# Optimization experiments

Hardware: AMD Instinct MI355X
Metric: run time of the kernel (lower is better)

The kernel has to match this reference:

```python
import jax, jax.numpy as jnp
import numpy as np


def setup_inputs() -> dict:
    key = jax.random.key(0)
    ks = jax.random.split(key, 8)
    B, E = 1024, 8
    dims = [480, 512, 512, 311]
    inp = {
        "x": jax.random.normal(ks[0], (B, dims[0]), dtype=jnp.float32),
        "weight_blend": jax.random.uniform(ks[1], (E, B), dtype=jnp.float32),
        "w0": jax.random.normal(ks[2], (E, dims[1], dims[0]), dtype=jnp.float32) * 0.05,
        "b0": jax.random.normal(ks[3], (E, dims[1]), dtype=jnp.float32) * 0.05,
        "w1": jax.random.normal(ks[4], (E, dims[2], dims[1]), dtype=jnp.float32) * 0.05,
        "b1": jax.random.normal(ks[5], (E, dims[2]), dtype=jnp.float32) * 0.05,
        "w2": jax.random.normal(ks[6], (E, dims[3], dims[2]), dtype=jnp.float32) * 0.05,
        "b2": jax.random.normal(ks[7], (E, dims[3]), dtype=jnp.float32) * 0.05,
    }
    return inp


def _blend_layer(h, blend, w, b):
    # Original: W_b = sum_e blend[e,b] * w[e]  (materializes [B, d_out, d_in]),
    # then matmul(W_b, h) + bias_b. Fused einsum computes identical math.
    out = jnp.einsum("eb,eoi,bi->bo", blend, w, h)
    out = out + jnp.einsum("eb,eo->bo", blend, b)
    return out


def reference(x, weight_blend, w0, b0, w1, b1, w2, b2):
    # dropout layers are identity (training=False / keep_prob=1)
    h = _blend_layer(x, weight_blend, w0, b0)
    h = jax.nn.elu(h)
    h = _blend_layer(h, weight_blend, w1, b1)
    h = jax.nn.elu(h)
    h = _blend_layer(h, weight_blend, w2, b2)  # no activation on final layer
    return h
```

## Files before the change

kernel.cpp:

```cpp
#include <hip/hip_runtime.h>

typedef __attribute__((ext_vector_type(8))) short short8;
typedef __attribute__((ext_vector_type(4))) float f32x4;

__device__ __forceinline__ unsigned short f2bf(float f) {
    unsigned u = __builtin_bit_cast(unsigned, f);
    unsigned r = (u + 0x7FFFu + ((u >> 16) & 1u)) >> 16;
    return (unsigned short)r;
}
__device__ __forceinline__ float bf2f(unsigned short u) {
    unsigned v = ((unsigned)u) << 16;
    return __builtin_bit_cast(float, v);
}

__device__ __forceinline__ void gload16(const unsigned short* g, unsigned short* l) {
    __builtin_amdgcn_global_load_lds(
        (const __attribute__((address_space(1))) void*)g,
        (__attribute__((address_space(3))) void*)l,
        16, 0, 0);
}

#define WAITV(N) asm volatile("s_waitcnt vmcnt(" #N ")" ::: "memory")
#define BAR() do { asm volatile("" ::: "memory"); __builtin_amdgcn_s_barrier(); asm volatile("" ::: "memory"); } while (0)

__device__ __forceinline__ short8 lds_read_swz(const unsigned short* tile, int row, int colb) {
    int off = row * 64 + colb;
    off ^= ((off >> 7) & 7) << 4;
    return *(const short8*)((const char*)tile + off);
}

__device__ __forceinline__ void cvt_chunk(const float* __restrict__ src,
                                          unsigned short* __restrict__ dst, int t) {
    const float4* s4 = (const float4*)src;
    float4 a = s4[2 * t], b = s4[2 * t + 1];
    union { unsigned short u[8]; int4 v; } r;
    r.u[0] = f2bf(a.x); r.u[1] = f2bf(a.y); r.u[2] = f2bf(a.z); r.u[3] = f2bf(a.w);
    r.u[4] = f2bf(b.x); r.u[5] = f2bf(b.y); r.u[6] = f2bf(b.z); r.u[7] = f2bf(b.w);
    ((int4*)dst)[t] = r.v;
}

__device__ __forceinline__ short8 pack8(float4 a, float4 b) {
    short8 p;
    p[0] = (short)f2bf(a.x); p[1] = (short)f2bf(a.y);
    p[2] = (short)f2bf(a.z); p[3] = (short)f2bf(a.w);
    p[4] = (short)f2bf(b.x); p[5] = (short)f2bf(b.y);
    p[6] = (short)f2bf(b.z); p[7] = (short)f2bf(b.w);
    return p;
}

__global__ __launch_bounds__(512) void k_gemm0(
    const float* __restrict__ A, const float* __restrict__ W,
    const float* __restrict__ blend, const float* __restrict__ bias,
    unsigned short* __restrict__ Y,
    const float* __restrict__ csrc, unsigned short* __restrict__ cdst)
{
    __shared__ unsigned short As[2][4096];
    __shared__ unsigned short Bs[2][4096];

    const int e  = blockIdx.z;
    const int bm = blockIdx.y * 128;
    const int on = blockIdx.x * 128;
    const int t  = threadIdx.x, lane = t & 63, w = t >> 6;
    const int wr = w >> 2, wc = w & 3;

    const int sr = lane >> 2, sce = (lane & 3) * 8;
    const int ra = w * 16 + sr;
    const float* gA = A + (size_t)(bm + ra) * 480 + sce;
    const float* gB = W + ((size_t)e * 512 + (on + ra)) * 480 + sce;

    int woff = ra * 64 + (lane & 3) * 16;
    woff ^= ((woff >> 7) & 7) << 4;

    float4 a0, a1, b0v, b1v;
    a0  = *(const float4*)(gA + 0); a1  = *(const float4*)(gA + 4);
    b0v = *(const float4*)(gB + 0); b1v = *(const float4*)(gB + 4);

    f32x4 acc[4][2] = {};

    for (int kt = 0; kt < 15; ++kt) {
        const int buf = kt & 1;
        *(short8*)((char*)As[buf] + woff) = pack8(a0, a1);
        *(short8*)((char*)Bs[buf] + woff) = pack8(b0v, b1v);
        __syncthreads();

        if (kt < 14) {
            int k0 = (kt + 1) * 32;
            a0  = *(const float4*)(gA + k0);     a1  = *(const float4*)(gA + k0 + 4);
            b0v = *(const float4*)(gB + k0);     b1v = *(const float4*)(gB + k0 + 4);
        }

        short8 af[4], bfr[2];
        #pragma unroll
        for (int fm = 0; fm < 4; ++fm)
            af[fm] = lds_read_swz(As[buf], wr * 64 + fm * 16 + (lane & 15), (lane >> 4) * 16);
        #pragma unroll
        for (int fn = 0; fn < 2; ++fn)
            bfr[fn] = lds_read_swz(Bs[buf], wc * 32 + fn * 16 + (lane & 15), (lane >> 4) * 16);
        #pragma unroll
        for (int fm = 0; fm < 4; ++fm)
            #pragma unroll
            for (int fn = 0; fn < 2; ++fn)
                acc[fm][fn] = __builtin_amdgcn_mfma_f32_16x16x32_bf16(
                    af[fm], bfr[fn], acc[fm][fn], 0, 0, 0);
        __syncthreads();
    }

    const float* blendE = blend + e * 1024;
    const float* biasE  = bias + (size_t)e * 512;
    unsigned short* Ye  = Y + (size_t)e * 1024 * 512;
    #pragma unroll
    for (int fm = 0; fm < 4; ++fm) {
        int i0 = bm + wr * 64 + fm * 16 + (lane >> 4) * 4;
        float4 bl = *(const float4*)&blendE[i0];
        #pragma unroll
        for (int fn = 0; fn < 2; ++fn) {
            int j = on + wc * 32 + fn * 16 + (lane & 15);
            float bs = biasE[j];
            #pragma unroll
            for (int r = 0; r < 4; ++r)
                Ye[(size_t)(i0 + r) * 512 + j] = f2bf((acc[fm][fn][r] + bs) * ((&bl.x)[r]));
        }
    }

    int lb = (blockIdx.z * 8 + blockIdx.y) * 4 + blockIdx.x;
    cvt_chunk(csrc, cdst, lb * 1024 + threadIdx.x);
    cvt_chunk(csrc, cdst, lb * 1024 + 512 + threadIdx.x);
}

__global__ __launch_bounds__(512) void k_gemm(
    const unsigned short* __restrict__ A,
    const unsigned short* __restrict__ W,
    const float* __restrict__ blend, const float* __restrict__ bias,
    unsigned short* __restrict__ Y,
    int K, int N, int ldy,
    const float* __restrict__ csrc, unsigned short* __restrict__ cdst, int nchunk)
{
    __shared__ unsigned short As[3][4096];
    __shared__ unsigned short Bs[3][4096];

    const int e  = blockIdx.z;
    const int bm = blockIdx.y * 128;
    const int on = blockIdx.x * 128;
    const int t  = threadIdx.x, lane = t & 63, w = t >> 6;
    const int wr = w >> 2, wc = w & 3;

    const unsigned short* Wt = W + (size_t)e * N * K;
    const int l2 = lane ^ ((lane >> 3) & 7);
    const int sr = l2 >> 2, sce = (l2 & 3) * 8;
    const int ra = w * 16 + sr;
    int rb = on + ra; if (rb > N - 1) rb = N - 1;
    const unsigned short* gA = A  + (size_t)(bm + ra) * K + sce;
    const unsigned short* gB = Wt + (size_t)rb * K + sce;

    const int ktn = K / 32;

#define STAGE(buf, kt) do { int _k0 = (kt) * 32;                       \
        gload16(gA + _k0, &As[(buf)][w * 512]);                        \
        gload16(gB + _k0, &Bs[(buf)][w * 512]); } while (0)

    f32x4 acc[4][2] = {};
    STAGE(0, 0); STAGE(1, 1); STAGE(2, 2);

    int cur = 0;
    for (int kt = 0; kt < ktn; ++kt) {
        int ahead = ktn - 1 - kt;
        if (ahead >= 2)      WAITV(4);
        else if (ahead == 1) WAITV(2);
        else                 WAITV(0);
        BAR();

        short8 af[4], bfr[2];
        #pragma unroll
        for (int fm = 0; fm < 4; ++fm)
            af[fm] = lds_read_swz(As[cur], wr * 64 + fm * 16 + (lane & 15), (lane >> 4) * 16);
        #pragma unroll
        for (int fn = 0; fn < 2; ++fn)
            bfr[fn] = lds_read_swz(Bs[cur], wc * 32 + fn * 16 + (lane & 15), (lane >> 4) * 16);
        #pragma unroll
        for (int fm = 0; fm < 4; ++fm)
            #pragma unroll
            for (int fn = 0; fn < 2; ++fn)
                acc[fm][fn] = __builtin_amdgcn_mfma_f32_16x16x32_bf16(
                    af[fm], bfr[fn], acc[fm][fn], 0, 0, 0);

        BAR();
        if (kt + 3 < ktn) STAGE(cur, kt + 3);
        cur = (cur == 2) ? 0 : cur + 1;
    }
#undef STAGE

    const float* blendE = blend + e * 1024;
    const float* biasE  = bias + (size_t)e * N;
    unsigned short* Ye  = Y + (size_t)e * 1024 * ldy;
    #pragma unroll
    for (int fm = 0; fm < 4; ++fm) {
        int i0 = bm + wr * 64 + fm * 16 + (lane >> 4) * 4;
        float4 bl = *(const float4*)&blendE[i0];
        #pragma unroll
        for (int fn = 0; fn < 2; ++fn) {
            int j = on + wc * 32 + fn * 16 + (lane & 15);
            if (j < N) {
                float bs = biasE[j];
                #pragma unroll
                for (int r = 0; r < 4; ++r)
                    Ye[(size_t)(i0 + r) * ldy + j] = f2bf((acc[fm][fn][r] + bs) * ((&bl.x)[r]));
            }
        }
    }

    if (cdst) {
        int lb = (blockIdx.z * 8 + blockIdx.y) * gridDim.x + blockIdx.x;
        #pragma unroll
        for (int q = 0; q < 2; ++q) {
            int tl = q * 512 + threadIdx.x;
            if (tl < nchunk) cvt_chunk(csrc, cdst, lb * nchunk + tl);
        }
    }
}

__global__ __launch_bounds__(256) void k_reduce8(
    const unsigned short* __restrict__ Y, unsigned short* __restrict__ out)
{
    int idx = blockIdx.x * 256 + threadIdx.x;
    int b  = idx >> 6;
    int o0 = (idx & 63) * 8;
    size_t base = (size_t)b * 512 + o0;
    float s[8] = {};
    #pragma unroll
    for (int p = 0; p < 8; ++p) {
        int4 v = *(const int4*)&Y[base + (size_t)p * 1024 * 512];
        const unsigned short* u = (const unsigned short*)&v;
        #pragma unroll
        for (int r = 0; r < 8; ++r) s[r] += bf2f(u[r]);
    }
    union { unsigned short u[8]; int4 v; } rr;
    #pragma unroll
    for (int r = 0; r < 8; ++r) {
        float v = (s[r] > 0.f) ? s[r] : expm1f(s[r]);
        rr.u[r] = f2bf(v);
    }
    *(int4*)&out[base] = rr.v;
}

__global__ __launch_bounds__(256) void k_reduce_last(
    const unsigned short* __restrict__ Y, float* __restrict__ out)
{
    int idx = blockIdx.x * 256 + threadIdx.x;
    if (idx >= 1024 * 40) return;
    int b  = idx / 40;
    int o0 = (idx - b * 40) * 8;
    size_t base = (size_t)b * 320 + o0;
    float s[8] = {};
    #pragma unroll
    for (int p = 0; p < 8; ++p) {
        int4 v = *(const int4*)&Y[base + (size_t)p * 1024 * 320];
        const unsigned short* u = (const unsigned short*)&v;
        #pragma unroll
        for (int r = 0; r < 8; ++r) s[r] += bf2f(u[r]);
    }
    #pragma unroll
    for (int r = 0; r < 8; ++r)
        if (o0 + r < 311) out[(size_t)b * 311 + o0 + r] = s[r];
}

extern "C" void kernel_launch(void* const* d_in, const int* in_sizes, int n_in,
                              void* d_out, int out_size, void* d_ws, size_t ws_size,
                              hipStream_t stream) {
    const float* x     = (const float*)d_in[0];
    const float* blend = (const float*)d_in[1];
    const float* w0    = (const float*)d_in[2];
    const float* b0    = (const float*)d_in[3];
    const float* w1    = (const float*)d_in[4];
    const float* b1    = (const float*)d_in[5];
    const float* w2    = (const float*)d_in[6];
    const float* b2    = (const float*)d_in[7];

    char* ws = (char*)d_ws;
    unsigned short* w1b = (unsigned short*)(ws + 0);
    unsigned short* w2b = (unsigned short*)(ws + 4194304);
    unsigned short* h1b = (unsigned short*)(ws + 6742016);
    unsigned short* h2b = (unsigned short*)(ws + 7790592);
    unsigned short* yb  = (unsigned short*)(ws + 8839168);

    k_gemm0<<<dim3(4, 8, 8), 512, 0, stream>>>(x, w0, blend, b0, yb, w1, w1b);
    k_reduce8<<<256, 256, 0, stream>>>(yb, h1b);

    k_gemm<<<dim3(4, 8, 8), 512, 0, stream>>>(h1b, w1b, blend, b1, yb, 512, 512, 512,
                                              w2, w2b, 622);
    k_reduce8<<<256, 256, 0, stream>>>(yb, h2b);

    k_gemm<<<dim3(3, 8, 8), 512, 0, stream>>>(h2b, w2b, blend, b2, yb, 512, 311, 320,
                                              nullptr, nullptr, 0);
    k_reduce_last<<<160, 256, 0, stream>>>(yb, (float*)d_out);
}
```

Baseline: 62.49 us.

## Deepen prefetch pipelines and drop a barrier per K-step in blended GEMMs

New measurement: 54.13 us. 13.4% less time.

```diff
diff --git a/kernel.cpp b/kernel.cpp
--- a/kernel.cpp
+++ b/kernel.cpp
@@ -21,6 +21,7 @@
 }
 
 #define WAITV(N) asm volatile("s_waitcnt vmcnt(" #N ")" ::: "memory")
+#define WAITL0() asm volatile("s_waitcnt lgkmcnt(0)" ::: "memory")
 #define BAR() do { asm volatile("" ::: "memory"); __builtin_amdgcn_s_barrier(); asm volatile("" ::: "memory"); } while (0)
 
 __device__ __forceinline__ short8 lds_read_swz(const unsigned short* tile, int row, int colb) {
@@ -71,24 +72,28 @@
     int woff = ra * 64 + (lane & 3) * 16;
     woff ^= ((woff >> 7) & 7) << 4;
 
-    float4 a0, a1, b0v, b1v;
-    a0  = *(const float4*)(gA + 0); a1  = *(const float4*)(gA + 4);
-    b0v = *(const float4*)(gB + 0); b1v = *(const float4*)(gB + 4);
+    float4 La0[3], La1[3], Lb0[3], Lb1[3];
+    #pragma unroll
+    for (int s = 0; s < 3; ++s) {
+        int k0 = s * 32;
+        La0[s] = *(const float4*)(gA + k0); La1[s] = *(const float4*)(gA + k0 + 4);
+        Lb0[s] = *(const float4*)(gB + k0); Lb1[s] = *(const float4*)(gB + k0 + 4);
+    }
 
     f32x4 acc[4][2] = {};
 
+    #pragma unroll
     for (int kt = 0; kt < 15; ++kt) {
-        const int buf = kt & 1;
-        *(short8*)((char*)As[buf] + woff) = pack8(a0, a1);
-        *(short8*)((char*)Bs[buf] + woff) = pack8(b0v, b1v);
-        __syncthreads();
-
-        if (kt < 14) {
-            int k0 = (kt + 1) * 32;
-            a0  = *(const float4*)(gA + k0);     a1  = *(const float4*)(gA + k0 + 4);
-            b0v = *(const float4*)(gB + k0);     b1v = *(const float4*)(gB + k0 + 4);
-        }
-
+        const int s = kt % 3, buf = kt & 1;
+        *(short8*)((char*)As[buf] + woff) = pack8(La0[s], La1[s]);
+        *(short8*)((char*)Bs[buf] + woff) = pack8(Lb0[s], Lb1[s]);
+        WAITL0();
+        BAR();
+        if (kt + 3 < 15) {
+            int k0 = (kt + 3) * 32;
+            La0[s] = *(const float4*)(gA + k0); La1[s] = *(const float4*)(gA + k0 + 4);
+            Lb0[s] = *(const float4*)(gB + k0); Lb1[s] = *(const float4*)(gB + k0 + 4);
+        }
         short8 af[4], bfr[2];
         #pragma unroll
         for (int fm = 0; fm < 4; ++fm)
@@ -102,7 +107,6 @@
             for (int fn = 0; fn < 2; ++fn)
                 acc[fm][fn] = __builtin_amdgcn_mfma_f32_16x16x32_bf16(
                     af[fm], bfr[fn], acc[fm][fn], 0, 0, 0);
-        __syncthreads();
     }
 
     const float* blendE = blend + e * 1024;
@@ -132,11 +136,11 @@
     const unsigned short* __restrict__ W,
     const float* __restrict__ blend, const float* __restrict__ bias,
     unsigned short* __restrict__ Y,
-    int K, int N, int ldy,
+    int N, int ldy,
     const float* __restrict__ csrc, unsigned short* __restrict__ cdst, int nchunk)
 {
-    __shared__ unsigned short As[3][4096];
-    __shared__ unsigned short Bs[3][4096];
+    __shared__ unsigned short As[4][4096];
+    __shared__ unsigned short Bs[4][4096];
 
     const int e  = blockIdx.z;
     const int bm = blockIdx.y * 128;
@@ -144,49 +148,46 @@
     const int t  = threadIdx.x, lane = t & 63, w = t >> 6;
     const int wr = w >> 2, wc = w & 3;
 
-    const unsigned short* Wt = W + (size_t)e * N * K;
+    const unsigned short* Wt = W + (size_t)e * N * 512;
     const int l2 = lane ^ ((lane >> 3) & 7);
     const int sr = l2 >> 2, sce = (l2 & 3) * 8;
     const int ra = w * 16 + sr;
     int rb = on + ra; if (rb > N - 1) rb = N - 1;
-    const unsigned short* gA = A  + (size_t)(bm + ra) * K + sce;
-    const unsigned short* gB = Wt + (size_t)rb * K + sce;
-
-    const int ktn = K / 32;
+    const unsigned short* gA = A  + (size_t)(bm + ra) * 512 + sce;
+    const unsigned short* gB = Wt + (size_t)rb * 512 + sce;
 
 #define STAGE(buf, kt) do { int _k0 = (kt) * 32;                       \
         gload16(gA + _k0, &As[(buf)][w * 512]);                        \
         gload16(gB + _k0, &Bs[(buf)][w * 512]); } while (0)
 
+#define COMPUTE(cur) do {                                                          \
+        short8 af[4], bfr[2];                                                      \
+        _Pragma("unroll")                                                          \
+        for (int fm = 0; fm < 4; ++fm)                                             \
+            af[fm] = lds_read_swz(As[(cur)], wr * 64 + fm * 16 + (lane & 15), (lane >> 4) * 16); \
+        _Pragma("unroll")                                                          \
+        for (int fn = 0; fn < 2; ++fn)                                             \
+            bfr[fn] = lds_read_swz(Bs[(cur)], wc * 32 + fn * 16 + (lane & 15), (lane >> 4) * 16); \
+        _Pragma("unroll")                                                          \
+        for (int fm = 0; fm < 4; ++fm)                                             \
+            _Pragma("unroll")                                                      \
+            for (int fn = 0; fn < 2; ++fn)                                         \
+                acc[fm][fn] = __builtin_amdgcn_mfma_f32_16x16x32_bf16(             \
+                    af[fm], bfr[fn], acc[fm][fn], 0, 0, 0);                        \
+    } while (0)
+
     f32x4 acc[4][2] = {};
     STAGE(0, 0); STAGE(1, 1); STAGE(2, 2);
 
-    int cur = 0;
-    for (int kt = 0; kt < ktn; ++kt) {
-        int ahead = ktn - 1 - kt;
-        if (ahead >= 2)      WAITV(4);
-        else if (ahead == 1) WAITV(2);
-        else                 WAITV(0);
+    for (int kt = 0; kt < 13; ++kt) {
+        WAITV(4);
         BAR();
-
-        short8 af[4], bfr[2];
-        #pragma unroll
-        for (int fm = 0; fm < 4; ++fm)
-            af[fm] = lds_read_swz(As[cur], wr * 64 + fm * 16 + (lane & 15), (lane >> 4) * 16);
-        #pragma unroll
-        for (int fn = 0; fn < 2; ++fn)
-            bfr[fn] = lds_read_swz(Bs[cur], wc * 32 + fn * 16 + (lane & 15), (lane >> 4) * 16);
-        #pragma unroll
-        for (int fm = 0; fm < 4; ++fm)
-            #pragma unroll
-            for (int fn = 0; fn < 2; ++fn)
-                acc[fm][fn] = __builtin_amdgcn_mfma_f32_16x16x32_bf16(
-                    af[fm], bfr[fn], acc[fm][fn], 0, 0, 0);
-
-        BAR();
-        if (kt + 3 < ktn) STAGE(cur, kt + 3);
-        cur = (cur == 2) ? 0 : cur + 1;
-    }
+        STAGE((kt + 3) & 3, kt + 3);
+        COMPUTE(kt & 3);
+    }
+    WAITV(4); BAR(); COMPUTE(1);
+    WAITV(2); BAR(); COMPUTE(2);
+    WAITV(0); BAR(); COMPUTE(3);
 #undef STAGE
 
     const float* blendE = blend + e * 1024;
@@ -285,11 +286,11 @@
     k_gemm0<<<dim3(4, 8, 8), 512, 0, stream>>>(x, w0, blend, b0, yb, w1, w1b);
     k_reduce8<<<256, 256, 0, stream>>>(yb, h1b);
 
-    k_gemm<<<dim3(4, 8, 8), 512, 0, stream>>>(h1b, w1b, blend, b1, yb, 512, 512, 512,
+    k_gemm<<<dim3(4, 8, 8), 512, 0, stream>>>(h1b, w1b, blend, b1, yb, 512, 512,
                                               w2, w2b, 622);
     k_reduce8<<<256, 256, 0, stream>>>(yb, h2b);
 
-    k_gemm<<<dim3(3, 8, 8), 512, 0, stream>>>(h2b, w2b, blend, b2, yb, 512, 311, 320,
+    k_gemm<<<dim3(3, 8, 8), 512, 0, stream>>>(h2b, w2b, blend, b2, yb, 311, 320,
                                               nullptr, nullptr, 0);
     k_reduce_last<<<160, 256, 0, stream>>>(yb, (float*)d_out);
 }
```
